# Optimization experiments

Hardware: AMD Instinct MI355X
Metric: run time of the kernel (lower is better)

Reference implementation:

```python
import jax, jax.numpy as jnp
import numpy as np

B, N, HID, H, M = 4, 16384, 512, 8, 32
D = HID // H  # 64


def setup_inputs() -> dict:
    key = jax.random.key(0)
    ks = jax.random.split(key, 8)
    s = 0.02
    return {
        "x": jax.random.normal(ks[0], (B, N, HID), jnp.float32),
        "wkv": jax.random.normal(ks[1], (2 * HID, HID), jnp.float32) * s,
        "bkv": jnp.zeros((2 * HID,), jnp.float32),
        "wtq": jax.random.normal(ks[2], (H, M, D), jnp.float32) * s,
        "alpha1": jnp.ones((H,), jnp.float32),
        "mix1_w": jax.random.normal(ks[3], (H * M, H * M), jnp.float32) * (1.0 / np.sqrt(H * M)),
        "ln1_w": jnp.ones((D,), jnp.float32),
        "ln1_b": jnp.zeros((D,), jnp.float32),
        "wqkv": jax.random.normal(ks[4], (3 * HID, HID), jnp.float32) * s,
        "wout": jax.random.normal(ks[5], (HID, HID), jnp.float32) * s,
        "bout": jnp.zeros((HID,), jnp.float32),
    }


def _layernorm(x, w, b, eps=1e-5):
    mu = x.mean(-1, keepdims=True)
    var = ((x - mu) ** 2).mean(-1, keepdims=True)
    return (x - mu) * jax.lax.rsqrt(var + eps) * w + b


def reference(x, wkv, bkv, wtq, alpha1, mix1_w, ln1_w, ln1_b, wqkv, wout, bout):
    # key/value projection: [B, N, 2*HID]
    kv = x @ wkv.T + bkv
    xk, xv = jnp.split(kv, 2, axis=-1)
    xk = xk.reshape(B, N, H, D).transpose(0, 2, 1, 3)  # b h n d
    xv = xv.reshape(B, N, H, D).transpose(0, 2, 1, 3)
    # slice scores + 1x1 conv head-mixing over the (H*M) channel dim
    scores = jnp.einsum('hmd,bhnd->bhmn', wtq, xk)
    scores = jnp.einsum('oc,bcn->bon', mix1_w, scores.reshape(B, H * M, N)).reshape(B, H, M, N)
    # softmax over the slice dim M (dim=-2)
    sw = jax.nn.softmax(scores * alpha1[:, None, None], axis=-2)  # b h m n
    # weighted reduction to slice tokens, normalized by total weight per slice
    tok = jnp.einsum('bhmn,bhnd->bhmd', sw, xv)
    tok = tok / (sw.sum(axis=-1, keepdims=True) + 1e-5)
    tok = _layernorm(tok, ln1_w, ln1_b)
    tok = tok.transpose(0, 2, 1, 3).reshape(B, M, HID)  # b m (h d)
    # small inner MHA over the M=32 slice tokens
    qkv = tok @ wqkv.T
    q, k, v = jnp.split(qkv, 3, axis=-1)
    q = q.reshape(B, M, H, D).transpose(0, 2, 1, 3)
    k = k.reshape(B, M, H, D).transpose(0, 2, 1, 3)
    v = v.reshape(B, M, H, D).transpose(0, 2, 1, 3)
    dots = jnp.einsum('bhqd,bhkd->bhqk', q, k) * (D ** -0.5)
    attn = jax.nn.softmax(dots, axis=-1)
    out_tok = jnp.einsum('bhqk,bhkd->bhqd', attn, v)
    # broadcast slice tokens back to the N points via slice weights
    out = jnp.einsum('bhmd,bhmn->bhnd', out_tok, sw)
    out = out.transpose(0, 2, 1, 3).reshape(B, N, HID)
    out = out @ wout.T + bout
    return (out, sw, alpha1[:, None, None], jnp.zeros((H, M), jnp.float32), attn)
```

## Files before the change

### kernel.cpp

```cpp
#include <hip/hip_runtime.h>
#include <hip/hip_bf16.h>

#define B_ 4
#define N_ 16384
#define HID_ 512
#define H_ 8
#define M_ 32
#define D_ 64
#define HM_ 256

typedef __hip_bfloat16 bf16;
typedef __bf16 bf16x8 __attribute__((ext_vector_type(8)));
typedef float f32x4 __attribute__((ext_vector_type(4)));

__device__ __forceinline__ void gl_lds16(const bf16* g, bf16* l) {
    __builtin_amdgcn_global_load_lds(
        (const __attribute__((address_space(1))) void*)g,
        (__attribute__((address_space(3))) void*)l, 16, 0, 0);
}

__device__ __forceinline__ int xcd_swz(int lin, int nwg) {
    return (lin & 7) * (nwg >> 3) + (lin >> 3);
}

__device__ __forceinline__ void stage_tile_lin(const bf16* __restrict__ G, long long r0,
        int kk, int ld, bf16* lds, int t) {
    const int l = t & 63, w = t >> 6;
    const int srow = l >> 3;
    const int skel = (l & 7) * 8;
#pragma unroll
    for (int j = 0; j < 4; ++j) {
        int q = j * 4 + w;
        gl_lds16(G + (r0 + q * 8 + srow) * (long long)ld + kk + skel, lds + q * 512);
    }
}

__device__ __forceinline__ void mfma_half(const bf16* As, const bf16* Bs,
        int l, int wm, int wn, f32x4 acc[4][4]) {
#pragma unroll
    for (int ks = 0; ks < 64; ks += 32) {
        bf16x8 af[4], bfr[4];
#pragma unroll
        for (int mf = 0; mf < 4; ++mf)
            af[mf] = *(const bf16x8*)(As + (wm * 64 + mf * 16 + (l & 15)) * 64 + ks + (l >> 4) * 8);
#pragma unroll
        for (int nf = 0; nf < 4; ++nf)
            bfr[nf] = *(const bf16x8*)(Bs + (wn * 64 + nf * 16 + (l & 15)) * 64 + ks + (l >> 4) * 8);
#pragma unroll
        for (int mf = 0; mf < 4; ++mf)
#pragma unroll
            for (int nf = 0; nf < 4; ++nf)
                acc[mf][nf] = __builtin_amdgcn_mfma_f32_16x16x32_bf16(af[mf], bfr[nf], acc[mf][nf], 0, 0, 0);
    }
}

__device__ __forceinline__ void mfma_core(
        const bf16* __restrict__ Ag, const bf16* __restrict__ Bg,
        long long arow0, int bcol0, int lda, int ldb, int kiters,
        bf16* As, bf16* Bs, f32x4 acc[4][4]) {
    const int t = threadIdx.x;
    const int l = t & 63, w = t >> 6;
    const int wm = w >> 1, wn = w & 1;
    for (int kt = 0; kt < kiters; ++kt) {
        const int kk = kt * 64;
        stage_tile_lin(Ag, arow0, kk, lda, As, t);
        stage_tile_lin(Bg, bcol0, kk, ldb, Bs, t);
        __syncthreads();
        mfma_half(As, Bs, l, wm, wn, acc);
        __syncthreads();
    }
}

template<int NT>
__device__ __forceinline__ void gemm_cnt(
        const bf16* __restrict__ Ag, const bf16* __restrict__ Bg,
        long long arow0, int bcol0, int lda, int ldb,
        bf16 (*As)[8192], bf16 (*Bs)[8192], f32x4 acc[4][4]) {
    const int t = threadIdx.x;
    const int l = t & 63, w = t >> 6;
    const int wm = w >> 1, wn = w & 1;
    stage_tile_lin(Ag, arow0, 0, lda, As[0], t);
    stage_tile_lin(Bg, bcol0, 0, ldb, Bs[0], t);
#pragma unroll
    for (int kt = 0; kt < NT; ++kt) {
        const int cur = kt & 1;
        if (kt + 1 < NT) {
            stage_tile_lin(Ag, arow0, (kt + 1) * 64, lda, As[cur ^ 1], t);
            stage_tile_lin(Bg, bcol0, (kt + 1) * 64, ldb, Bs[cur ^ 1], t);
            asm volatile("s_waitcnt vmcnt(8)" ::: "memory");
        } else {
            asm volatile("s_waitcnt vmcnt(0)" ::: "memory");
        }
        __builtin_amdgcn_s_barrier();
        mfma_half(As[cur], Bs[cur], l, wm, wn, acc);
        __builtin_amdgcn_s_barrier();
    }
}

__global__ __launch_bounds__(256) void k_cast4(const float* __restrict__ s,
        ushort* __restrict__ d) {
    long long i = (long long)blockIdx.x * 256 + threadIdx.x;
    float4 v = reinterpret_cast<const float4*>(s)[i];
    ushort4 o;
    bf16 a0 = __float2bfloat16(v.x), a1 = __float2bfloat16(v.y);
    bf16 a2 = __float2bfloat16(v.z), a3 = __float2bfloat16(v.w);
    o.x = *(ushort*)&a0; o.y = *(ushort*)&a1; o.z = *(ushort*)&a2; o.w = *(ushort*)&a3;
    reinterpret_cast<ushort4*>(d)[i] = o;
}

__global__ __launch_bounds__(256) void k_wfused(const float* __restrict__ mix1,
        const float* __restrict__ wtq, float* __restrict__ wf) {
    const int idx = blockIdx.x * 256 + threadIdx.x;
    const int o = idx >> 9, k = idx & 511;
    const int h = k >> 6, dd = k & 63;
    float s = 0.f;
#pragma unroll
    for (int m = 0; m < 32; ++m)
        s += mix1[(long long)o * 256 + h * 32 + m] * wtq[((long long)h * 32 + m) * 64 + dd];
    wf[(long long)o * 512 + k] = s;
}

__global__ __launch_bounds__(256) void k_wsc(const float* __restrict__ wf,
        const float* __restrict__ wkv, const float* __restrict__ bkv,
        const float* __restrict__ alpha1, bf16* __restrict__ wv_sc,
        float* __restrict__ bias768) {
    __shared__ float wfrow[512];
    __shared__ float red[256];
    const int o = blockIdx.x, t = threadIdx.x;
    wfrow[t] = wf[(long long)o * 512 + t];
    wfrow[t + 256] = wf[(long long)o * 512 + 256 + t];
    __syncthreads();
    const float al = alpha1[o >> 5];
    float a0 = 0.f, a1 = 0.f;
    for (int c = 0; c < 512; ++c) {
        float wv = wfrow[c];
        a0 += wv * wkv[(long long)c * 512 + t];
        a1 += wv * wkv[(long long)c * 512 + t + 256];
    }
    wv_sc[(long long)(512 + o) * 512 + t] = __float2bfloat16(a0 * al);
    wv_sc[(long long)(512 + o) * 512 + t + 256] = __float2bfloat16(a1 * al);
    float p = wfrow[t] * bkv[t] + wfrow[t + 256] * bkv[t + 256];
    red[t] = p; __syncthreads();
    for (int s = 128; s >= 1; s >>= 1) {
        if (t < s) red[t] += red[t + s];
        __syncthreads();
    }
    if (t == 0) bias768[512 + o] = red[0] * al;
    if (t < 2) bias768[o * 2 + t] = bkv[512 + o * 2 + t];
}

__global__ __launch_bounds__(256) void k12_mfma(const bf16* __restrict__ xb,
        const bf16* __restrict__ wv_sc, const float* __restrict__ bias768,
        bf16* __restrict__ xv, float* __restrict__ swout,
        bf16* __restrict__ sw_bt, float* __restrict__ part) {
    __shared__ __align__(16) bf16 As[2][8192];
    __shared__ __align__(16) bf16 Bs[2][8192];
    f32x4 acc[4][4];
#pragma unroll
    for (int i = 0; i < 4; ++i)
#pragma unroll
        for (int j = 0; j < 4; ++j) acc[i][j] = (f32x4)(0.0f);
    const int wg = xcd_swz(blockIdx.y * 6 + blockIdx.x, 3072);
    const int bx = wg % 6, by = wg / 6;
    const long long arow0 = (long long)by * 128;
    const int bcol0 = bx * 128;
    gemm_cnt<8>(xb, wv_sc, arow0, bcol0, 512, 512, As, Bs, acc);

    const int t = threadIdx.x;
    const int l = t & 63, w = t >> 6, wm = w >> 1, wn = w & 1;
    const int l15 = l & 15, lq = l >> 4;
#pragma unroll
    for (int nf = 0; nf < 4; ++nf) {
        float bv = bias768[bcol0 + wn * 64 + nf * 16 + l15];
#pragma unroll
        for (int mf = 0; mf < 4; ++mf)
#pragma unroll
            for (int r = 0; r < 4; ++r) acc[mf][nf][r] += bv;
    }

    if (bcol0 >= 512) {
#pragma unroll
        for (int mf = 0; mf < 4; ++mf)
#pragma unroll
            for (int r = 0; r < 4; ++r)
#pragma unroll
                for (int g = 0; g < 2; ++g) {
                    float v0 = acc[mf][2 * g][r], v1 = acc[mf][2 * g + 1][r];
                    float mx = fmaxf(v0, v1);
#pragma unroll
                    for (int mk = 1; mk <= 8; mk <<= 1) mx = fmaxf(mx, __shfl_xor(mx, mk));
                    float e0 = __expf(v0 - mx), e1 = __expf(v1 - mx);
                    float s = e0 + e1;
#pragma unroll
                    for (int mk = 1; mk <= 8; mk <<= 1) s += __shfl_xor(s, mk);
                    float ri = 1.f / s;
                    acc[mf][2 * g][r] = e0 * ri;
                    acc[mf][2 * g + 1][r] = e1 * ri;
                }
        {
            float* cpart = (float*)&As[0][0];
#pragma unroll
            for (int nf = 0; nf < 4; ++nf) {
                float ps = 0.f;
#pragma unroll
                for (int mf = 0; mf < 4; ++mf)
#pragma unroll
                    for (int r = 0; r < 4; ++r) ps += acc[mf][nf][r];
                ps += __shfl_xor(ps, 16);
                ps += __shfl_xor(ps, 32);
                if (lq == 0) cpart[wm * 128 + wn * 64 + nf * 16 + l15] = ps;
            }
            __syncthreads();
            if (t < 128)
                part[(long long)by * 256 + (bcol0 - 512) + t] = cpart[t] + cpart[128 + t];
        }
        const int b = (int)(arow0 >> 14);
        const int nbase = (int)(arow0 & 16383) + wm * 64;
#pragma unroll
        for (int mf = 0; mf < 4; ++mf) {
            long long rowb = arow0 + wm * 64 + mf * 16 + lq * 4;
#pragma unroll
            for (int nf = 0; nf < 4; ++nf) {
                int cglob = (bcol0 - 512) + wn * 64 + nf * 16 + l15;
                float4 v = {acc[mf][nf][0], acc[mf][nf][1], acc[mf][nf][2], acc[mf][nf][3]};
                *reinterpret_cast<float4*>(swout + ((long long)b * HM_ + cglob) * N_
                                           + nbase + mf * 16 + lq * 4) = v;
#pragma unroll
                for (int r = 0; r < 4; ++r)
                    sw_bt[(rowb + r) * 256 + cglob] = __float2bfloat16(acc[mf][nf][r]);
            }
        }
    } else {
#pragma unroll
        for (int mf = 0; mf < 4; ++mf) {
            long long rowb = arow0 + wm * 64 + mf * 16 + lq * 4;
#pragma unroll
            for (int nf = 0; nf < 4; ++nf) {
                int col = bcol0 + wn * 64 + nf * 16 + l15;
#pragma unroll
                for (int r = 0; r < 4; ++r)
                    xv[(rowb + r) * 512 + col] = __float2bfloat16(acc[mf][nf][r]);
            }
        }
    }
}

__global__ __launch_bounds__(256) void k3_tok(const bf16* __restrict__ sw_bt,
        const bf16* __restrict__ xv, float* __restrict__ tok_part) {
    __shared__ __align__(16) float smem[17408];
    float (*swsT)[36] = reinterpret_cast<float(*)[36]>(smem);
    bf16* xvs = reinterpret_cast<bf16*>(smem + 9216);
    const int t = threadIdx.x;
    const int chunk = blockIdx.x;
    const int bh = blockIdx.y;
    const int n0 = chunk * 256;
    const int b = bh >> 3, h = bh & 7;
    {
        const long long base = ((long long)(b * N_ + n0 + t)) * 256 + h * 32;
        const uint4* sp = reinterpret_cast<const uint4*>(sw_bt + base);
        uint4 qs[4] = {sp[0], sp[1], sp[2], sp[3]};
        const uint* qu = reinterpret_cast<const uint*>(qs);
#pragma unroll
        for (int j = 0; j < 16; ++j) {
            uint u = qu[j];
            swsT[t][2 * j] = __uint_as_float(u << 16);
            swsT[t][2 * j + 1] = __uint_as_float(u & 0xffff0000u);
        }
    }
    {
        const uint* xg = reinterpret_cast<const uint*>(xv + ((long long)b * N_ + n0) * 512 + h * 64);
        uint* xls = reinterpret_cast<uint*>(xvs);
#pragma unroll
        for (int p = 0; p < 32; ++p) {
            int idx = p * 256 + t;
            int nl = idx >> 5, prt = idx & 31;
            xls[nl * 32 + prt] = xg[(long long)nl * 256 + prt];
        }
    }
    __syncthreads();
    const int l = t & 63, w = t >> 6;
    const int nlh = l >> 5, mtile = (l >> 3) & 3, dtile = l & 7;
    const int m0 = mtile * 8, d0 = dtile * 8;
    float acc[8][8] = {};
    const int wbase = w * 64;
    for (int i = 0; i < 32; ++i) {
        int nl = wbase + i * 2 + nlh;
        float4 s0 = *reinterpret_cast<const float4*>(&swsT[nl][m0]);
        float4 s1 = *reinterpret_cast<const float4*>(&swsT[nl][m0 + 4]);
        uint4 xi = *reinterpret_cast<const uint4*>(&xvs[nl * 64 + d0]);
        float xvf[8];
        xvf[0] = __uint_as_float(xi.x << 16); xvf[1] = __uint_as_float(xi.x & 0xffff0000u);
        xvf[2] = __uint_as_float(xi.y << 16); xvf[3] = __uint_as_float(xi.y & 0xffff0000u);
        xvf[4] = __uint_as_float(xi.z << 16); xvf[5] = __uint_as_float(xi.z & 0xffff0000u);
        xvf[6] = __uint_as_float(xi.w << 16); xvf[7] = __uint_as_float(xi.w & 0xffff0000u);
        float sm[8] = {s0.x, s0.y, s0.z, s0.w, s1.x, s1.y, s1.z, s1.w};
#pragma unroll
        for (int mi = 0; mi < 8; ++mi)
#pragma unroll
            for (int di = 0; di < 8; ++di)
                acc[mi][di] += sm[mi] * xvf[di];
    }
    __syncthreads();
    float* red = smem;
    float* rb = red + (w * 2 + nlh) * 2048;
#pragma unroll
    for (int mi = 0; mi < 8; ++mi) {
        float4 lo = {acc[mi][0], acc[mi][1], acc[mi][2], acc[mi][3]};
        float4 hi = {acc[mi][4], acc[mi][5], acc[mi][6], acc[mi][7]};
        *reinterpret_cast<float4*>(&rb[(m0 + mi) * 64 + d0]) = lo;
        *reinterpret_cast<float4*>(&rb[(m0 + mi) * 64 + d0 + 4]) = hi;
    }
    __syncthreads();
#pragma unroll
    for (int pp = 0; pp < 2; ++pp) {
        int idx4 = pp * 1024 + t * 4;
        float4 s = {0.f, 0.f, 0.f, 0.f};
#pragma unroll
        for (int r = 0; r < 8; ++r) {
            float4 v = *reinterpret_cast<const float4*>(&red[r * 2048 + idx4]);
            s.x += v.x; s.y += v.y; s.z += v.z; s.w += v.w;
        }
        *reinterpret_cast<float4*>(&tok_part[((long long)bh * 64 + chunk) * 2048 + idx4]) = s;
    }
}

__global__ __launch_bounds__(64) void k4a_ln(const float* __restrict__ tok_part,
        const float* __restrict__ part, const float* __restrict__ ln_w,
        const float* __restrict__ ln_b, float* __restrict__ tok_ln) {
    const int bid = blockIdx.x;
    const int bh = bid >> 5, m = bid & 31;
    const int d = threadIdx.x;
    float s = 0.f;
    for (int ch = 0; ch < 64; ++ch)
        s += tok_part[(((long long)bh * 64 + ch) * 32 + m) * 64 + d];
    const int b = bid >> 8, c = bid & 255;
    float ssum = part[((long long)(b * 128 + d)) * 256 + c]
               + part[((long long)(b * 128 + 64 + d)) * 256 + c];
#pragma unroll
    for (int mk = 32; mk >= 1; mk >>= 1) ssum += __shfl_xor(ssum, mk, 64);
    float tokv = s / (ssum + 1e-5f);
    float mu = tokv;
#pragma unroll
    for (int mk = 32; mk >= 1; mk >>= 1) mu += __shfl_xor(mu, mk, 64);
    mu *= (1.f / 64.f);
    float df = tokv - mu;
    float var = df * df;
#pragma unroll
    for (int mk = 32; mk >= 1; mk >>= 1) var += __shfl_xor(var, mk, 64);
    var *= (1.f / 64.f);
    float y = df * rsqrtf(var + 1e-5f) * ln_w[d] + ln_b[d];
    const int bb = bh >> 3, h = bh & 7;
    tok_ln[((long long)bb * 32 + m) * 512 + h * 64 + d] = y;
}

__global__ __launch_bounds__(256) void k_wqT(const float* __restrict__ wq,
        float* __restrict__ wqT) {
    __shared__ float tile[32][33];
    const int k0 = blockIdx.x * 32;
    const int j0 = blockIdx.y * 32;
    const int tx = threadIdx.x & 31, ty = threadIdx.x >> 5;
#pragma unroll
    for (int r = 0; r < 32; r += 8)
        tile[ty + r][tx] = wq[(long long)(j0 + ty + r) * 512 + k0 + tx];
    __syncthreads();
#pragma unroll
    for (int r = 0; r < 32; r += 8)
        wqT[(long long)(k0 + ty + r) * 1536 + j0 + tx] = tile[tx][ty + r];
}

__global__ __launch_bounds__(256) void k4b_qkv(const float* __restrict__ tok_ln,
        const float* __restrict__ wqT, float* __restrict__ qkv) {
    const int j = (blockIdx.x % 6) * 256 + threadIdx.x;
    const int r0 = (blockIdx.x / 6) * 4;
    float a0 = 0, a1 = 0, a2 = 0, a3 = 0;
    for (int k = 0; k < 512; ++k) {
        float wv = wqT[(long long)k * 1536 + j];
        a0 += tok_ln[(r0 + 0) * 512 + k] * wv;
        a1 += tok_ln[(r0 + 1) * 512 + k] * wv;
        a2 += tok_ln[(r0 + 2) * 512 + k] * wv;
        a3 += tok_ln[(r0 + 3) * 512 + k] * wv;
    }
    qkv[(long long)(r0 + 0) * 1536 + j] = a0;
    qkv[(long long)(r0 + 1) * 1536 + j] = a1;
    qkv[(long long)(r0 + 2) * 1536 + j] = a2;
    qkv[(long long)(r0 + 3) * 1536 + j] = a3;
}

__global__ __launch_bounds__(256) void k4c_attn(const float* __restrict__ qkv,
        float* __restrict__ out_tok, float* __restrict__ attn_out) {
    __shared__ float qsT[64][33], ksT[64][33], vsT[64][33];
    __shared__ float att[32][33];
    __shared__ float rinv[32];
    const int t = threadIdx.x;
    const int bid = blockIdx.x;
    const int b = bid >> 3, h = bid & 7;
#pragma unroll
    for (int i = 0; i < 8; ++i) {
        int idx = i * 256 + t;
        int mi = idx >> 6, dd = idx & 63;
        long long base = ((long long)b * 32 + mi) * 1536 + h * 64 + dd;
        qsT[dd][mi] = qkv[base];
        ksT[dd][mi] = qkv[base + 512];
        vsT[dd][mi] = qkv[base + 1024];
    }
    __syncthreads();
#pragma unroll
    for (int i = 0; i < 4; ++i) {
        int idx = i * 256 + t;
        int qi = idx >> 5, ki = idx & 31;
        float s = 0.f;
#pragma unroll
        for (int dd = 0; dd < 64; ++dd) s += qsT[dd][qi] * ksT[dd][ki];
        att[qi][ki] = s * 0.125f;
    }
    __syncthreads();
    if (t < 32) {
        float mx = -1e30f;
        for (int k = 0; k < 32; ++k) mx = fmaxf(mx, att[t][k]);
        float sum = 0.f;
        for (int k = 0; k < 32; ++k) { float e = __expf(att[t][k] - mx); att[t][k] = e; sum += e; }
        rinv[t] = 1.f / sum;
    }
    __syncthreads();
#pragma unroll
    for (int i = 0; i < 4; ++i) {
        int idx = i * 256 + t;
        int qi = idx >> 5, ki = idx & 31;
        float a = att[qi][ki] * rinv[qi];
        att[qi][ki] = a;
        attn_out[(long long)bid * 1024 + qi * 32 + ki] = a;
    }
    __syncthreads();
#pragma unroll
    for (int i = 0; i < 8; ++i) {
        int idx = i * 256 + t;
        int qi = idx >> 6, dd = idx & 63;
        float s = 0.f;
#pragma unroll
        for (int ki = 0; ki < 32; ++ki) s += att[qi][ki] * vsT[dd][ki];
        out_tok[((long long)bid * 32 + qi) * 64 + dd] = s;
    }
}

__global__ __launch_bounds__(256) void k5_w2(const float* __restrict__ wout,
        const float* __restrict__ out_tok, bf16* __restrict__ W2) {
    const int bid = blockIdx.x;
    const int b = bid >> 9, o = bid & 511;
    const int t = threadIdx.x;
    const int h = t >> 5, m = t & 31;
    float s = 0.f;
#pragma unroll
    for (int dd = 0; dd < 64; ++dd)
        s += wout[(long long)o * 512 + h * 64 + dd]
           * out_tok[(((long long)b * 8 + h) * 32 + m) * 64 + dd];
    W2[(long long)bid * 256 + t] = __float2bfloat16(s);
}

__global__ __launch_bounds__(256) void k6_mfma(const bf16* __restrict__ sw_bt,
        const bf16* __restrict__ W2, const float* __restrict__ bout,
        float* __restrict__ out) {
    __shared__ bf16 As[128 * 64], Bs[128 * 64];
    f32x4 acc[4][4];
#pragma unroll
    for (int i = 0; i < 4; ++i)
#pragma unroll
        for (int j = 0; j < 4; ++j) acc[i][j] = (f32x4)(0.0f);
    const int wg = xcd_swz((blockIdx.z * 128 + blockIdx.y) * 4 + blockIdx.x, 2048);
    const int bx = wg & 3, by = (wg >> 2) & 127, bz = wg >> 9;
    const long long arow0 = (long long)by * 128;
    const int bcol0 = bx * 128;
    mfma_core(sw_bt + (long long)bz * N_ * 256, W2 + (long long)bz * 512 * 256,
              arow0, bcol0, 256, 256, 4, As, Bs, acc);
    const int l = threadIdx.x & 63, w = threadIdx.x >> 6;
    const int wm = w >> 1, wn = w & 1;
#pragma unroll
    for (int mf = 0; mf < 4; ++mf) {
#pragma unroll
        for (int nf = 0; nf < 4; ++nf) {
            int col = bcol0 + wn * 64 + nf * 16 + (l & 15);
            float bv = bout[col];
#pragma unroll
            for (int r = 0; r < 4; ++r) {
                long long row = arow0 + wm * 64 + mf * 16 + (l >> 4) * 4 + r;
                out[((long long)bz * N_ + row) * 512 + col] = acc[mf][nf][r] + bv;
            }
        }
    }
}

__global__ void k_misc(const float* __restrict__ alpha1,
        float* __restrict__ outA, float* __restrict__ outZ) {
    int t = threadIdx.x;
    if (t < 8) outA[t] = alpha1[t];
    outZ[t] = 0.f;
}

extern "C" void kernel_launch(void* const* d_in, const int* in_sizes, int n_in,
                              void* d_out, int out_size, void* d_ws, size_t ws_size,
                              hipStream_t stream) {
    const float* x      = (const float*)d_in[0];
    const float* wkv    = (const float*)d_in[1];
    const float* bkv    = (const float*)d_in[2];
    const float* wtq    = (const float*)d_in[3];
    const float* alpha1 = (const float*)d_in[4];
    const float* mix1_w = (const float*)d_in[5];
    const float* ln1_w  = (const float*)d_in[6];
    const float* ln1_b  = (const float*)d_in[7];
    const float* wqkv   = (const float*)d_in[8];
    const float* wout   = (const float*)d_in[9];
    const float* bout   = (const float*)d_in[10];

    float* out    = (float*)d_out;
    float* swout  = out + 33554432LL;
    float* alphaO = out + 50331648LL;
    float* zerosO = out + 50331656LL;
    float* attnO  = out + 50331912LL;

    char* ws = (char*)d_ws;
    bf16*  xb        = (bf16*)(ws);
    float* wqkvT     = (float*)(ws);
    float* wf_f32    = (float*)(ws + 35651584LL);
    float* part      = (float*)(ws + 67108864LL);
    bf16*  sw_bt     = (bf16*)(ws + 100663296LL);
    bf16*  xv        = (bf16*)(ws + 134217728LL);
    float* tok_part  = (float*)(ws + 201326592LL);
    float* tok_ln    = (float*)(ws + 218107904LL);
    float* qkv       = (float*)(ws + 218370048LL);
    float* out_tok   = (float*)(ws + 219156480LL);
    bf16*  W2b       = (bf16*)(ws + 219418624LL);
    bf16*  wv_sc     = (bf16*)(ws + 220467200LL);
    float* bias768   = (float*)(ws + 221253632LL);

    k_cast4<<<256, 256, 0, stream>>>(wkv + 262144, (ushort*)wv_sc);
    k_wfused<<<512, 256, 0, stream>>>(mix1_w, wtq, wf_f32);
    k_wsc<<<256, 256, 0, stream>>>(wf_f32, wkv, bkv, alpha1, wv_sc, bias768);
    k_cast4<<<32768, 256, 0, stream>>>(x, (ushort*)xb);
    k12_mfma<<<dim3(6, 512), 256, 0, stream>>>(xb, wv_sc, bias768, xv, swout, sw_bt, part);
    k_wqT<<<dim3(16, 48), 256, 0, stream>>>(wqkv, wqkvT);
    k3_tok<<<dim3(64, 32), 256, 0, stream>>>(sw_bt, xv, tok_part);
    k4a_ln<<<1024, 64, 0, stream>>>(tok_part, part, ln1_w, ln1_b, tok_ln);
    k4b_qkv<<<192, 256, 0, stream>>>(tok_ln, wqkvT, qkv);
    k4c_attn<<<32, 256, 0, stream>>>(qkv, out_tok, attnO);
    k5_w2<<<2048, 256, 0, stream>>>(wout, out_tok, W2b);
    k6_mfma<<<dim3(4, 128, 4), 256, 0, stream>>>(sw_bt, W2b, bout, out);
    k_misc<<<1, 256, 0, stream>>>(alpha1, alphaO, zerosO);
}
```

Measured before the change: 343.8 us.

## Halve GEMM K-tile to 32 and move fp32 sw output to separate transpose kernel

The k12 GEMM K-step drops from 64 to 32, halving LDS use per block, presumably so more blocks fit per CU. The fp32 softmax-weight output is no longer written from the GEMM epilogue. A new k_swT kernel reads the bf16 sw_bt buffer, transposes it through shared memory, and writes coalesced float4 rows. This lightens the GEMM epilogue at the cost of an extra launch and another read of sw_bt, and the fp32 sw output now carries bf16 precision.

Measured after the change: 355.7 us. 1.03x slower.

```diff
diff --git a/kernel.cpp b/kernel.cpp
--- a/kernel.cpp
+++ b/kernel.cpp
@@ -35,6 +35,18 @@
     }
 }
 
+__device__ __forceinline__ void stage_tile32(const bf16* __restrict__ G, long long r0,
+        int kk, int ld, bf16* lds, int t) {
+    const int l = t & 63, w = t >> 6;
+    const int srow = l >> 2;
+    const int scol = (l & 3) * 8;
+#pragma unroll
+    for (int j = 0; j < 2; ++j) {
+        int q = j * 4 + w;
+        gl_lds16(G + (r0 + q * 16 + srow) * (long long)ld + kk + scol, lds + q * 512);
+    }
+}
+
 __device__ __forceinline__ void mfma_half(const bf16* As, const bf16* Bs,
         int l, int wm, int wn, f32x4 acc[4][4]) {
 #pragma unroll
@@ -52,6 +64,23 @@
             for (int nf = 0; nf < 4; ++nf)
                 acc[mf][nf] = __builtin_amdgcn_mfma_f32_16x16x32_bf16(af[mf], bfr[nf], acc[mf][nf], 0, 0, 0);
     }
+}
+
+__device__ __forceinline__ void mfma_half32(const bf16* As, const bf16* Bs,
+        int l, int wm, int wn, f32x4 acc[4][4]) {
+    const int l15 = l & 15, kq = (l >> 4) * 8;
+    bf16x8 af[4], bfr[4];
+#pragma unroll
+    for (int mf = 0; mf < 4; ++mf)
+        af[mf] = *(const bf16x8*)(As + (wm * 64 + mf * 16 + l15) * 32 + kq);
+#pragma unroll
+    for (int nf = 0; nf < 4; ++nf)
+        bfr[nf] = *(const bf16x8*)(Bs + (wn * 64 + nf * 16 + l15) * 32 + kq);
+#pragma unroll
+    for (int mf = 0; mf < 4; ++mf)
+#pragma unroll
+        for (int nf = 0; nf < 4; ++nf)
+            acc[mf][nf] = __builtin_amdgcn_mfma_f32_16x16x32_bf16(af[mf], bfr[nf], acc[mf][nf], 0, 0, 0);
 }
 
 __device__ __forceinline__ void mfma_core(
@@ -72,27 +101,27 @@
 }
 
 template<int NT>
-__device__ __forceinline__ void gemm_cnt(
+__device__ __forceinline__ void gemm_cnt32(
         const bf16* __restrict__ Ag, const bf16* __restrict__ Bg,
         long long arow0, int bcol0, int lda, int ldb,
-        bf16 (*As)[8192], bf16 (*Bs)[8192], f32x4 acc[4][4]) {
+        bf16 (*As)[4096], bf16 (*Bs)[4096], f32x4 acc[4][4]) {
     const int t = threadIdx.x;
     const int l = t & 63, w = t >> 6;
     const int wm = w >> 1, wn = w & 1;
-    stage_tile_lin(Ag, arow0, 0, lda, As[0], t);
-    stage_tile_lin(Bg, bcol0, 0, ldb, Bs[0], t);
+    stage_tile32(Ag, arow0, 0, lda, As[0], t);
+    stage_tile32(Bg, bcol0, 0, ldb, Bs[0], t);
 #pragma unroll
     for (int kt = 0; kt < NT; ++kt) {
         const int cur = kt & 1;
         if (kt + 1 < NT) {
-            stage_tile_lin(Ag, arow0, (kt + 1) * 64, lda, As[cur ^ 1], t);
-            stage_tile_lin(Bg, bcol0, (kt + 1) * 64, ldb, Bs[cur ^ 1], t);
-            asm volatile("s_waitcnt vmcnt(8)" ::: "memory");
+            stage_tile32(Ag, arow0, (kt + 1) * 32, lda, As[cur ^ 1], t);
+            stage_tile32(Bg, bcol0, (kt + 1) * 32, ldb, Bs[cur ^ 1], t);
+            asm volatile("s_waitcnt vmcnt(4)" ::: "memory");
         } else {
             asm volatile("s_waitcnt vmcnt(0)" ::: "memory");
         }
         __builtin_amdgcn_s_barrier();
-        mfma_half(As[cur], Bs[cur], l, wm, wn, acc);
+        mfma_half32(As[cur], Bs[cur], l, wm, wn, acc);
         __builtin_amdgcn_s_barrier();
     }
 }
@@ -151,10 +180,9 @@
 
 __global__ __launch_bounds__(256) void k12_mfma(const bf16* __restrict__ xb,
         const bf16* __restrict__ wv_sc, const float* __restrict__ bias768,
-        bf16* __restrict__ xv, float* __restrict__ swout,
-        bf16* __restrict__ sw_bt, float* __restrict__ part) {
-    __shared__ __align__(16) bf16 As[2][8192];
-    __shared__ __align__(16) bf16 Bs[2][8192];
+        bf16* __restrict__ xv, bf16* __restrict__ sw_bt, float* __restrict__ part) {
+    __shared__ __align__(16) bf16 As[2][4096];
+    __shared__ __align__(16) bf16 Bs[2][4096];
     f32x4 acc[4][4];
 #pragma unroll
     for (int i = 0; i < 4; ++i)
@@ -164,7 +192,7 @@
     const int bx = wg % 6, by = wg / 6;
     const long long arow0 = (long long)by * 128;
     const int bcol0 = bx * 128;
-    gemm_cnt<8>(xb, wv_sc, arow0, bcol0, 512, 512, As, Bs, acc);
+    gemm_cnt32<16>(xb, wv_sc, arow0, bcol0, 512, 512, As, Bs, acc);
 
     const int t = threadIdx.x;
     const int l = t & 63, w = t >> 6, wm = w >> 1, wn = w & 1;
@@ -214,17 +242,12 @@
             if (t < 128)
                 part[(long long)by * 256 + (bcol0 - 512) + t] = cpart[t] + cpart[128 + t];
         }
-        const int b = (int)(arow0 >> 14);
-        const int nbase = (int)(arow0 & 16383) + wm * 64;
 #pragma unroll
         for (int mf = 0; mf < 4; ++mf) {
             long long rowb = arow0 + wm * 64 + mf * 16 + lq * 4;
 #pragma unroll
             for (int nf = 0; nf < 4; ++nf) {
                 int cglob = (bcol0 - 512) + wn * 64 + nf * 16 + l15;
-                float4 v = {acc[mf][nf][0], acc[mf][nf][1], acc[mf][nf][2], acc[mf][nf][3]};
-                *reinterpret_cast<float4*>(swout + ((long long)b * HM_ + cglob) * N_
-                                           + nbase + mf * 16 + lq * 4) = v;
 #pragma unroll
                 for (int r = 0; r < 4; ++r)
                     sw_bt[(rowb + r) * 256 + cglob] = __float2bfloat16(acc[mf][nf][r]);
@@ -242,6 +265,34 @@
                     xv[(rowb + r) * 512 + col] = __float2bfloat16(acc[mf][nf][r]);
             }
         }
+    }
+}
+
+__global__ __launch_bounds__(256) void k_swT(const bf16* __restrict__ sw_bt,
+        float* __restrict__ swout) {
+    __shared__ float T[256][33];
+    const int t = threadIdx.x;
+    const int n0 = blockIdx.x * 256;
+    const int bc = blockIdx.y;
+    const int b = bc >> 3, cg = bc & 7;
+    const uint4* src = reinterpret_cast<const uint4*>(
+        sw_bt + ((long long)(b * N_ + n0 + t)) * 256 + cg * 32);
+    uint4 q0 = src[0], q1 = src[1], q2 = src[2], q3 = src[3];
+    uint qu[16] = {q0.x, q0.y, q0.z, q0.w, q1.x, q1.y, q1.z, q1.w,
+                   q2.x, q2.y, q2.z, q2.w, q3.x, q3.y, q3.z, q3.w};
+#pragma unroll
+    for (int j = 0; j < 16; ++j) {
+        T[t][2 * j] = __uint_as_float(qu[j] << 16);
+        T[t][2 * j + 1] = __uint_as_float(qu[j] & 0xffff0000u);
+    }
+    __syncthreads();
+    const int c = t >> 3, ng = t & 7;
+    float* dst = swout + ((long long)b * HM_ + cg * 32 + c) * N_ + n0 + ng * 32;
+#pragma unroll
+    for (int i = 0; i < 8; ++i) {
+        int nb = ng * 32 + i * 4;
+        float4 v = {T[nb][c], T[nb + 1][c], T[nb + 2][c], T[nb + 3][c]};
+        *reinterpret_cast<float4*>(dst + i * 4) = v;
     }
 }
 
@@ -535,7 +586,8 @@
     k_wfused<<<512, 256, 0, stream>>>(mix1_w, wtq, wf_f32);
     k_wsc<<<256, 256, 0, stream>>>(wf_f32, wkv, bkv, alpha1, wv_sc, bias768);
     k_cast4<<<32768, 256, 0, stream>>>(x, (ushort*)xb);
-    k12_mfma<<<dim3(6, 512), 256, 0, stream>>>(xb, wv_sc, bias768, xv, swout, sw_bt, part);
+    k12_mfma<<<dim3(6, 512), 256, 0, stream>>>(xb, wv_sc, bias768, xv, sw_bt, part);
+    k_swT<<<dim3(64, 32), 256, 0, stream>>>(sw_bt, swout);
     k_wqT<<<dim3(16, 48), 256, 0, stream>>>(wqkv, wqkvT);
     k3_tok<<<dim3(64, 32), 256, 0, stream>>>(sw_bt, xv, tok_part);
     k4a_ln<<<1024, 64, 0, stream>>>(tok_part, part, ln1_w, ln1_b, tok_ln);
```
